# Kernel tuning notes

Measured on AMD Instinct MI355X. Metric: run time of the kernel, lower is better.

The kernel has to match this reference:

```python
import jax, jax.numpy as jnp
import numpy as np
from jax import lax

M, T, WINDOW = 4096, 2048, 25
NEG_DIAG = -1e10  # matches alphas.fill_diagonal_(-1e10)


def setup_inputs() -> dict:
    key = jax.random.key(0)
    k_ys, k_a, k_r, k_b0, k_b1 = jax.random.split(key, 5)
    ys = jax.random.uniform(k_ys, (M, T), dtype=jnp.float32) * 10.0  # case counts
    alphas = 0.01 * jax.random.normal(k_a, (M, M), dtype=jnp.float32)
    repro = 1.0 + 0.01 * jax.random.normal(k_r, (M, WINDOW), dtype=jnp.float32)  # init ones
    b0 = 0.1 * jax.random.normal(k_b0, (M, 1), dtype=jnp.float32)
    b1 = 0.01 * jax.random.normal(k_b1, (M, 1), dtype=jnp.float32)
    t = jnp.arange(T, dtype=jnp.int32) + 1
    return {"ys": ys, "alphas": alphas, "repro": repro, "b0": b0, "b1": b1, "t": t}


def reference(ys, alphas, repro, b0, b1, t):
    m, _ = ys.shape
    window = repro.shape[1]
    offset = window - 1
    # metapopulation weights: sigmoid adjacency with diagonal forced to ~0
    diag = jnp.eye(m, dtype=bool)
    W = jax.nn.sigmoid(jnp.where(diag, jnp.asarray(NEG_DIAG, ys.dtype), alphas))
    # depthwise conv1d (cross-correlation), groups=M, VALID padding -> (M, T-window+1)
    Z = lax.conv_general_dilated(
        ys[None],                 # (1, M, T)
        repro[:, None, :],        # (M, 1, window)
        window_strides=(1,),
        padding='VALID',
        feature_group_count=m,
        dimension_numbers=('NCH', 'OIH', 'NCH'),
    )[0]                          # (M, T')
    ys_n = ys[:, offset:]         # (M, T')
    # beta_net: per-node softplus-linear in time -> (M, T), then narrow
    tt = t.astype(ys.dtype)
    beta = jax.nn.softplus(b0 + b1 * tt[None, :])[:, offset:]  # (M, T')
    return beta * (jax.nn.softplus(Z) + W @ ys_n)
```

## Files before the change

kernel.cpp:

```cpp
#include <hip/hip_runtime.h>
#include <stdint.h>

#define M_DIM 4096
#define T_DIM 2048
#define N_OUT 2024
#define N_PAD 2048
#define WIN   25
#define K_DIM 4096

typedef float f32x4 __attribute__((ext_vector_type(4)));

__device__ __forceinline__ unsigned short f2bf(float x) {
  unsigned u = __float_as_uint(x);
  u += 0x7FFF + ((u >> 16) & 1);
  return (unsigned short)(u >> 16);
}
__device__ __forceinline__ float bf2f(unsigned short h) {
  return __uint_as_float(((unsigned)h) << 16);
}

__device__ __forceinline__ void gl2lds16(const void* g, void* l) {
  __builtin_amdgcn_global_load_lds(
      (const __attribute__((address_space(1))) unsigned int*)g,
      (__attribute__((address_space(3))) unsigned int*)l, 16, 0, 0);
}

__device__ __forceinline__ int pk_fp8x4(float a, float b, float c, float d) {
  int w = __builtin_amdgcn_cvt_pk_fp8_f32(a, b, 0, false);
  w = __builtin_amdgcn_cvt_pk_fp8_f32(c, d, w, true);
  return w;
}

__global__ __launch_bounds__(256) void k_wcast(const float* __restrict__ alphas,
                                               unsigned char* __restrict__ W8) {
  size_t i8 = ((size_t)blockIdx.x * 256 + threadIdx.x) * 8;
  const float4 v0 = *(const float4*)(alphas + i8);
  const float4 v1 = *(const float4*)(alphas + i8 + 4);
  int row = (int)(i8 >> 12);
  int col = (int)(i8 & 4095);
  float a[8] = {v0.x, v0.y, v0.z, v0.w, v1.x, v1.y, v1.z, v1.w};
  float w[8];
#pragma unroll
  for (int j = 0; j < 8; ++j)
    w[j] = (row == col + j) ? 0.f : 1.f / (1.f + __expf(-a[j]));
  int p0 = pk_fp8x4(w[0], w[1], w[2], w[3]);
  int p1 = pk_fp8x4(w[4], w[5], w[6], w[7]);
  *(uint2*)(W8 + i8) = uint2{(unsigned)p0, (unsigned)p1};
}

__global__ __launch_bounds__(256) void k_conv(const float* __restrict__ ys,
                                              const float* __restrict__ repro,
                                              unsigned short* __restrict__ Sbf) {
  __shared__ float sy[256 + WIN - 1];
  __shared__ float sr[WIN];
  int m = blockIdx.y;
  int j0 = blockIdx.x * 256;
  int tid = threadIdx.x;
  sy[tid] = ys[(size_t)m * T_DIM + j0 + tid];
  if (tid < WIN - 1) {
    int jj = j0 + 256 + tid;
    sy[256 + tid] = (jj < T_DIM) ? ys[(size_t)m * T_DIM + jj] : 0.f;
  }
  if (tid < WIN) sr[tid] = repro[m * WIN + tid];
  __syncthreads();
  int j = j0 + tid;
  float z = 0.f;
#pragma unroll
  for (int k = 0; k < WIN; ++k) z += sy[tid + k] * sr[k];
  float sp = fmaxf(z, 0.f) + log1pf(__expf(-fabsf(z)));
  Sbf[(size_t)m * N_PAD + j] = (j < N_OUT) ? f2bf(sp) : (unsigned short)0;
}

__global__ __launch_bounds__(256) void k_transpose(const float* __restrict__ ys,
                                                   unsigned char* __restrict__ BT8) {
  __shared__ float t[64][65];
  int n0 = blockIdx.x * 64;
  int k0 = blockIdx.y * 64;
  int tx = threadIdx.x;
  int ty = threadIdx.y;
#pragma unroll
  for (int r = 0; r < 16; ++r) {
    int kk = k0 + ty + r * 4;
    int n = n0 + tx;
    t[ty + r * 4][tx] = (n < N_OUT) ? ys[(size_t)kk * T_DIM + n + (WIN - 1)] : 0.f;
  }
  __syncthreads();
  int tid = ty * 64 + tx;
  int nl = tid >> 2;
  int kc = (tid & 3) * 16;
  unsigned wds[4];
#pragma unroll
  for (int w = 0; w < 4; ++w)
    wds[w] = (unsigned)pk_fp8x4(t[kc + 4 * w][nl], t[kc + 4 * w + 1][nl],
                                t[kc + 4 * w + 2][nl], t[kc + 4 * w + 3][nl]);
  *(uint4*)(BT8 + (size_t)(n0 + nl) * K_DIM + k0 + kc) =
      uint4{wds[0], wds[1], wds[2], wds[3]};
}

__global__ __launch_bounds__(256) void k_gemm(const unsigned char* __restrict__ W8,
                                              const unsigned char* __restrict__ BT8,
                                              const unsigned short* __restrict__ Sbf,
                                              const float* __restrict__ b0,
                                              const float* __restrict__ b1,
                                              float* __restrict__ out) {
  __shared__ __align__(16) unsigned char lA[128 * 64];
  __shared__ __align__(16) unsigned char lB[128 * 64];
  const int tid  = threadIdx.x;
  const int wave = tid >> 6;
  const int lane = tid & 63;
  const int wm = wave >> 1, wn = wave & 1;
  const int m16  = lane & 15;
  const int quad = lane >> 4;
  const int tileM = blockIdx.y * 128;
  const int tileN = blockIdx.x * 128;

  const int key  = (m16 >> 1) & 3;
  const int sub  = (quad & 1) * 8;
  const int rowA = (wm * 64 + m16) * 64;
  const int rowB = (wn * 64 + m16) * 64;
  int hOf[2];
#pragma unroll
  for (int h = 0; h < 2; ++h)
    hOf[h] = (((2 * h + (quad >> 1)) ^ key) << 4) + sub;

  const unsigned char* gA[2];
  const unsigned char* gB[2];
  unsigned char* ldsA[2];
  unsigned char* ldsB[2];
#pragma unroll
  for (int c = 0; c < 2; ++c) {
    int o  = c * 4096 + wave * 1024 + lane * 16;
    int r  = o >> 6;
    int s  = (o >> 4) & 3;
    int q  = s ^ ((r >> 1) & 3);
    gA[c] = W8  + (size_t)(tileM + r) * K_DIM + q * 16;
    gB[c] = BT8 + (size_t)(tileN + r) * K_DIM + q * 16;
    ldsA[c] = lA + c * 4096 + wave * 1024;
    ldsB[c] = lB + c * 4096 + wave * 1024;
  }

  f32x4 acc[4][4];
#pragma unroll
  for (int i = 0; i < 4; ++i)
#pragma unroll
    for (int j = 0; j < 4; ++j) acc[i][j] = f32x4{0.f, 0.f, 0.f, 0.f};

  for (int kt = 0; kt < K_DIM / 64; ++kt) {
    const size_t kb = (size_t)kt * 64;
#pragma unroll
    for (int c = 0; c < 2; ++c) {
      gl2lds16(gA[c] + kb, ldsA[c]);
      gl2lds16(gB[c] + kb, ldsB[c]);
    }
    __syncthreads();
#pragma unroll
    for (int h = 0; h < 2; ++h) {
      long long aF[4], bF[4];
#pragma unroll
      for (int i = 0; i < 4; ++i) {
        aF[i] = *(const long long*)(lA + rowA + i * 1024 + hOf[h]);
        bF[i] = *(const long long*)(lB + rowB + i * 1024 + hOf[h]);
      }
#pragma unroll
      for (int i = 0; i < 4; ++i)
#pragma unroll
        for (int j = 0; j < 4; ++j)
          acc[i][j] = __builtin_amdgcn_mfma_f32_16x16x32_fp8_fp8(
              aF[i], bF[j], acc[i][j], 0, 0, 0);
    }
    __syncthreads();
  }

#pragma unroll
  for (int j = 0; j < 4; ++j) {
    int gn = tileN + wn * 64 + j * 16 + m16;
    if (gn >= N_OUT) continue;
    float tval = (float)(gn + WIN);
#pragma unroll
    for (int i = 0; i < 4; ++i) {
#pragma unroll
      for (int r = 0; r < 4; ++r) {
        int gm = tileM + wm * 64 + i * 16 + quad * 4 + r;
        float x = b0[gm] + b1[gm] * tval;
        float beta = fmaxf(x, 0.f) + log1pf(__expf(-fabsf(x)));
        float s = bf2f(Sbf[(size_t)gm * N_PAD + gn]);
        out[(size_t)gm * N_OUT + gn] = beta * (s + acc[i][j][r]);
      }
    }
  }
}

extern "C" void kernel_launch(void* const* d_in, const int* in_sizes, int n_in,
                              void* d_out, int out_size, void* d_ws, size_t ws_size,
                              hipStream_t stream) {
  const float* ys     = (const float*)d_in[0];
  const float* alphas = (const float*)d_in[1];
  const float* repro  = (const float*)d_in[2];
  const float* b0     = (const float*)d_in[3];
  const float* b1     = (const float*)d_in[4];
  float* out = (float*)d_out;

  char* ws = (char*)d_ws;
  unsigned char*  W8  = (unsigned char*)ws;
  unsigned char*  BT8 = (unsigned char*)(ws + (size_t)M_DIM * K_DIM);
  unsigned short* Sbf = (unsigned short*)(ws + (size_t)M_DIM * K_DIM
                                             + (size_t)N_PAD * K_DIM);

  k_wcast<<<(M_DIM * (size_t)K_DIM) / 8 / 256, 256, 0, stream>>>(alphas, W8);
  k_conv<<<dim3(T_DIM / 256, M_DIM), 256, 0, stream>>>(ys, repro, Sbf);
  k_transpose<<<dim3(N_PAD / 64, K_DIM / 64), dim3(64, 4), 0, stream>>>(ys, BT8);
  k_gemm<<<dim3(N_PAD / 128, M_DIM / 128), 256, 0, stream>>>(W8, BT8, Sbf, b0, b1, out);
}
```

Measured before the change: 263.9 us.

## Pipeline GEMM global-to-LDS loads with four-stage LDS ring buffer

Replaces the single-buffered LDS tile in the fp8 GEMM with a four-slot ring and keeps two tiles in flight ahead of compute, using explicit vmcnt waits and barriers. This is meant to hide global load latency behind MFMA work instead of stalling on each tile. LDS use grows from 16KB to 64KB per block, which can lower occupancy. The hand-tuned waitcnt counts must match the number of outstanding loads.

```diff
diff --git a/kernel.cpp b/kernel.cpp
--- a/kernel.cpp
+++ b/kernel.cpp
@@ -103,8 +103,8 @@
                                               const float* __restrict__ b0,
                                               const float* __restrict__ b1,
                                               float* __restrict__ out) {
-  __shared__ __align__(16) unsigned char lA[128 * 64];
-  __shared__ __align__(16) unsigned char lB[128 * 64];
+  __shared__ __align__(64) unsigned char lA[4][128 * 64];
+  __shared__ __align__(64) unsigned char lB[4][128 * 64];
   const int tid  = threadIdx.x;
   const int wave = tid >> 6;
   const int lane = tid & 63;
@@ -125,8 +125,7 @@
 
   const unsigned char* gA[2];
   const unsigned char* gB[2];
-  unsigned char* ldsA[2];
-  unsigned char* ldsB[2];
+  int ldsOff[2];
 #pragma unroll
   for (int c = 0; c < 2; ++c) {
     int o  = c * 4096 + wave * 1024 + lane * 16;
@@ -135,8 +134,7 @@
     int q  = s ^ ((r >> 1) & 3);
     gA[c] = W8  + (size_t)(tileM + r) * K_DIM + q * 16;
     gB[c] = BT8 + (size_t)(tileN + r) * K_DIM + q * 16;
-    ldsA[c] = lA + c * 4096 + wave * 1024;
-    ldsB[c] = lB + c * 4096 + wave * 1024;
+    ldsOff[c] = c * 4096 + wave * 1024;
   }
 
   f32x4 acc[4][4];
@@ -145,21 +143,22 @@
 #pragma unroll
     for (int j = 0; j < 4; ++j) acc[i][j] = f32x4{0.f, 0.f, 0.f, 0.f};
 
-  for (int kt = 0; kt < K_DIM / 64; ++kt) {
-    const size_t kb = (size_t)kt * 64;
+  auto stage = [&](int buf, int kt_) {
+    const size_t kb_ = (size_t)kt_ * 64;
 #pragma unroll
     for (int c = 0; c < 2; ++c) {
-      gl2lds16(gA[c] + kb, ldsA[c]);
-      gl2lds16(gB[c] + kb, ldsB[c]);
-    }
-    __syncthreads();
+      gl2lds16(gA[c] + kb_, &lA[buf][ldsOff[c]]);
+      gl2lds16(gB[c] + kb_, &lB[buf][ldsOff[c]]);
+    }
+  };
+  auto compute = [&](int buf) {
 #pragma unroll
     for (int h = 0; h < 2; ++h) {
       long long aF[4], bF[4];
 #pragma unroll
       for (int i = 0; i < 4; ++i) {
-        aF[i] = *(const long long*)(lA + rowA + i * 1024 + hOf[h]);
-        bF[i] = *(const long long*)(lB + rowB + i * 1024 + hOf[h]);
+        aF[i] = *(const long long*)&lA[buf][rowA + i * 1024 + hOf[h]];
+        bF[i] = *(const long long*)&lB[buf][rowB + i * 1024 + hOf[h]];
       }
 #pragma unroll
       for (int i = 0; i < 4; ++i)
@@ -168,7 +167,52 @@
           acc[i][j] = __builtin_amdgcn_mfma_f32_16x16x32_fp8_fp8(
               aF[i], bF[j], acc[i][j], 0, 0, 0);
     }
-    __syncthreads();
+  };
+
+  stage(0, 0);
+  stage(1, 1);
+
+#pragma unroll 1
+  for (int kt = 0; kt < K_DIM / 64; kt += 4) {
+    stage(2, kt + 2);
+    asm volatile("s_waitcnt vmcnt(8)" ::: "memory");
+    __builtin_amdgcn_s_barrier();
+    asm volatile("" ::: "memory");
+    compute(0);
+    __builtin_amdgcn_s_barrier();
+    asm volatile("" ::: "memory");
+
+    stage(3, kt + 3);
+    asm volatile("s_waitcnt vmcnt(8)" ::: "memory");
+    __builtin_amdgcn_s_barrier();
+    asm volatile("" ::: "memory");
+    compute(1);
+    __builtin_amdgcn_s_barrier();
+    asm volatile("" ::: "memory");
+
+    if (kt + 4 < K_DIM / 64) {
+      stage(0, kt + 4);
+      asm volatile("s_waitcnt vmcnt(8)" ::: "memory");
+    } else {
+      asm volatile("s_waitcnt vmcnt(4)" ::: "memory");
+    }
+    __builtin_amdgcn_s_barrier();
+    asm volatile("" ::: "memory");
+    compute(2);
+    __builtin_amdgcn_s_barrier();
+    asm volatile("" ::: "memory");
+
+    if (kt + 5 < K_DIM / 64) {
+      stage(1, kt + 5);
+      asm volatile("s_waitcnt vmcnt(8)" ::: "memory");
+    } else {
+      asm volatile("s_waitcnt vmcnt(0)" ::: "memory");
+    }
+    __builtin_amdgcn_s_barrier();
+    asm volatile("" ::: "memory");
+    compute(3);
+    __builtin_amdgcn_s_barrier();
+    asm volatile("" ::: "memory");
   }
 
 #pragma unroll
```

Result: faster. 258.8 us (-2.0%).
